# Kernel tuning notes

Hardware: AMD Instinct MI355X
Metric: run time of the kernel (lower is better)

The kernel has to match this reference:

```python
import jax, jax.numpy as jnp
import numpy as np


def _next_pow2(n: int) -> int:
    # matches torch: 2 ** ceil(log2(n))
    return 1 << (int(n) - 1).bit_length()


def setup_inputs() -> dict:
    key = jax.random.key(0)
    k1, k2 = jax.random.split(key)
    B, T, L = 256, 32768, 32768
    x = jax.random.normal(k1, (B, T), dtype=jnp.float32)
    filt = jax.random.normal(k2, (1, L), dtype=jnp.float32)
    return {"x": x, "filt": filt}


def reference(x, filt):
    """EpochedFutureFill.forward: exact causal convolution of x with filt.

    The per-token epoched algorithm (tau-step direct sum + FutureFill FFT
    cache refresh every K steps, cache initialized to zero) computes exactly
    y[b, t] = sum_{s=0}^{min(t, L-1)} filt[0, s] * x[b, t-s].
    We compute it with one FFT-based linear convolution, mirroring the
    float32 FFT math of future_fill().
    """
    B, T = x.shape
    L = filt.shape[-1]
    n_fft = _next_pow2(T + L - 1)
    xf = jnp.fft.rfft(x.astype(jnp.float32), n=n_fft)          # (B, n_fft//2+1)
    wf = jnp.fft.rfft(filt.astype(jnp.float32), n=n_fft)       # (1, n_fft//2+1)
    y = jnp.fft.irfft(xf * wf, n=n_fft)[:, :T]                 # causal lags 0..T-1
    return y.astype(x.dtype)
```

## Files before the change

### kernel.cpp

```cpp
#include <hip/hip_runtime.h>
#include <cstdint>

typedef __attribute__((ext_vector_type(8))) short short8;
typedef __attribute__((ext_vector_type(4))) float floatx4;

#define TWO_PI 6.283185307179586f

__device__ __forceinline__ unsigned short f2bf(float f) {
  union { float f; uint32_t u; } c; c.f = f;
  uint32_t u = c.u;
  u += 0x7FFFu + ((u >> 16) & 1u);
  return (unsigned short)(u >> 16);
}
__device__ __forceinline__ uint32_t packbf(float re, float im) {
  return (uint32_t)f2bf(re) | ((uint32_t)f2bf(im) << 16);
}


__global__ __launch_bounds__(256) void prep_all(
    const float* __restrict__ x, const float* __restrict__ filt,
    unsigned short* __restrict__ A1, unsigned short* __restrict__ A2,
    unsigned short* __restrict__ A3, unsigned short* __restrict__ A4,
    uint32_t* __restrict__ Zp, float2* __restrict__ Gw,
    float2* __restrict__ Tw) {
  __shared__ float2 roots[256];
  const int bid = blockIdx.x;
  const int tid = threadIdx.x;
  const float w256 = TWO_PI / 256.0f;
  if (bid < 3072) {
    if (bid < 512) {
      int j = bid * 256 + tid;
      int jj = j & 7, ln = (j >> 3) & 63, ks = (j >> 9) & 1;
      int t = j >> 10, M16 = t & 31, kc = t >> 5;
      int row = M16 * 16 + (ln & 15);
      int col = kc * 64 + ks * 32 + (ln >> 4) * 8 + jj;
      int k1 = row >> 1, d = row & 1, r = col >> 1, e = col & 1;
      float th = (float)((k1 * r) & 255) * w256;
      float sn, cs; __sincosf(th, &sn, &cs);
      A1[j] = f2bf(d == 0 ? (e == 0 ? cs : sn) : (e == 0 ? -sn : cs));
    } else if (bid < 1536) {
      int j = (bid - 512) * 256 + tid;
      int jj = j & 7, ln = (j >> 3) & 63, ks = (j >> 9) & 1;
      int t = j >> 10, M16 = t & 31, kc = t >> 5;
      int row = M16 * 16 + (ln & 15);
      int col = kc * 64 + ks * 32 + (ln >> 4) * 8 + jj;
      int k2 = row >> 1, d = row & 1, cc = col >> 1, e = col & 1;
      float th = (float)((k2 * cc) & 255) * w256;
      float sn, cs; __sincosf(th, &sn, &cs);
      A2[j] = f2bf(d == 0 ? (e == 0 ? cs : sn) : (e == 0 ? -sn : cs));
    } else if (bid < 2560) {
      int j = (bid - 1536) * 256 + tid;
      int jj = j & 7, ln = (j >> 3) & 63, ks = (j >> 9) & 1;
      int t = j >> 10, M16 = t & 31, kc = t >> 5;
      int row = M16 * 16 + (ln & 15);
      int col = kc * 64 + ks * 32 + (ln >> 4) * 8 + jj;
      int cc = row >> 1, d = row & 1, k2 = col >> 1, e = col & 1;
      float th = (float)((k2 * cc) & 255) * w256;
      float sn, cs; __sincosf(th, &sn, &cs);
      A3[j] = f2bf(d == 0 ? (e == 0 ? cs : -sn) : (e == 0 ? sn : cs));
    } else {
      int j = (bid - 2560) * 256 + tid;
      int jj = j & 7, ln = (j >> 3) & 63, ks = (j >> 9) & 1;
      int t = j >> 10, M16 = t & 15, kc = t >> 4;
      int row = M16 * 16 + (ln & 15);
      int col = kc * 64 + ks * 32 + (ln >> 4) * 8 + jj;
      int r = row >> 1, d = row & 1, k1 = col >> 1, e = col & 1;
      float th = (float)((k1 * r) & 255) * w256;
      float sn, cs; __sincosf(th, &sn, &cs);
      A4[j] = f2bf(d == 0 ? (e == 0 ? cs : -sn) : (e == 0 ? sn : cs));
    }
  } else if (bid < 4096) {
    int b2 = bid - 3072;
    int s = b2 >> 3, rq = b2 & 7;
    const float* x0 = x + (size_t)(2 * s) * 32768;
    const float* x1 = x0 + 32768;
    uint32_t v[16];
    #pragma unroll
    for (int rr = 0; rr < 16; ++rr) {
      int t = tid + 256 * (rq * 16 + rr);
      v[rr] = (uint32_t)f2bf(x0[t]) | ((uint32_t)f2bf(x1[t]) << 16);
    }
    const int kc = rq >> 1, ks = rq & 1;
    uint32_t* dst = Zp + (size_t)s * 32768 +
                    ((kc * 16 + (tid >> 4)) * 2 + ks) * 256 + (tid & 15) * 4;
    #pragma unroll
    for (int q = 0; q < 4; ++q)
      *(uint4*)(dst + q * 64) = make_uint4(v[4*q], v[4*q+1], v[4*q+2], v[4*q+3]);
  } else if (bid < 4352) {
    int k1 = bid - 4096, c = tid;
    { float sn, cs; __sincosf((float)tid * w256, &sn, &cs);
      roots[tid] = make_float2(cs, sn); }
    __syncthreads();
    float ar = 0.f, ai = 0.f;
    for (int r = 0; r < 128; ++r) {
      float v = filt[c + 256 * r];
      float2 wv = roots[(k1 * r) & 255];
      ar += v * wv.x; ai -= v * wv.y;
    }
    float th = (float)((k1 * c) & 65535) * (TWO_PI / 65536.0f);
    float sn, cs; __sincosf(th, &sn, &cs);
    Gw[(k1 << 8) + c] = make_float2(ar * cs + ai * sn, ai * cs - ar * sn);
  } else {
    int k1 = bid - 4352, c = tid;
    float th = (float)((k1 * c) & 65535) * (TWO_PI / 65536.0f);
    float sn, cs; __sincosf(th, &sn, &cs);
    Tw[(k1 << 8) + c] = make_float2(cs, sn);
  }
}

__global__ __launch_bounds__(256) void prep_wb(const float2* __restrict__ Gw,
                                               float2* __restrict__ WtT) {
  __shared__ float2 roots[256];
  int k1 = blockIdx.x, k2 = threadIdx.x;
  { float sn, cs; __sincosf((float)k2 * (TWO_PI / 256.0f), &sn, &cs);
    roots[k2] = make_float2(cs, sn); }
  __syncthreads();
  float ar = 0.f, ai = 0.f;
  for (int c = 0; c < 256; ++c) {
    float2 g = Gw[(k1 << 8) + c];
    float2 wv = roots[(k2 * c) & 255];
    ar += g.x * wv.x + g.y * wv.y;
    ai += g.y * wv.x - g.x * wv.y;
  }
  WtT[(k2 << 8) + k1] = make_float2(ar, ai);
}

template <int MODE, int KC, int MD16>
__global__ __launch_bounds__(256, 2) void dft_stageR(
    const unsigned short* __restrict__ Af,
    const uint32_t* __restrict__ Bf,
    uint32_t* __restrict__ outp,
    float* __restrict__ yout,
    const float2* __restrict__ tab) {
  __shared__ uint32_t Tr[(MODE == 4) ? 64 : 8704];

  const int mt = blockIdx.x >> 8;
  const int nt = blockIdx.x & 255;
  const int m0 = mt * 128, n0 = nt * 128;
  const int s = n0 >> 8;
  const int nlow = n0 & 255;

  const int tid = threadIdx.x;
  const int w = tid >> 6, lane = tid & 63;
  const int qlo = lane & 15, qhi = lane >> 4;
  const int wr = w >> 1, wc = w & 1;

  floatx4 acc[4][4];
  #pragma unroll
  for (int i = 0; i < 4; ++i)
    #pragma unroll
    for (int j = 0; j < 4; ++j) acc[i][j] = (floatx4){0.f, 0.f, 0.f, 0.f};

  const uint32_t* Bp = Bf + (size_t)s * (KC * 8192);
  const int m16b = (m0 >> 4) + wr * 4;
  const int n16b = (nlow >> 4) + wc * 4;

  #pragma unroll
  for (int kc = 0; kc < KC; ++kc) {
    #pragma unroll
    for (int ks = 0; ks < 2; ++ks) {
      short8 a[4], b[4];
      #pragma unroll
      for (int im = 0; im < 4; ++im)
        a[im] = *(const short8*)(Af +
            (size_t)(((kc * MD16 + m16b + im) * 2 + ks) * 512 + lane * 8));
      #pragma unroll
      for (int in = 0; in < 4; ++in)
        b[in] = *(const short8*)(Bp +
            (((kc * 16 + n16b + in) * 2 + ks) * 256 + lane * 4));
      #pragma unroll
      for (int im = 0; im < 4; ++im)
        #pragma unroll
        for (int in = 0; in < 4; ++in)
          acc[im][in] = __builtin_amdgcn_mfma_f32_16x16x32_bf16(
              a[im], b[in], acc[im][in], 0, 0, 0);
    }
  }

  if constexpr (MODE == 1) {
    #pragma unroll
    for (int im = 0; im < 4; ++im) {
      const int mloc = wr * 32 + im * 8 + qhi * 2;
      #pragma unroll
      for (int in = 0; in < 4; ++in) {
        const int nloc = wc * 64 + in * 16 + qlo;
        const int c = nlow + nloc;
        #pragma unroll
        for (int pp = 0; pp < 2; ++pp) {
          const int k1loc = mloc + pp;
          const int k1 = (m0 >> 1) + k1loc;
          float re = acc[im][in][2*pp], iv = acc[im][in][2*pp+1];
          float2 tw = tab[(k1 << 8) + c];
          float r2 = re * tw.x + iv * tw.y, i2 = iv * tw.x - re * tw.y;
          Tr[k1loc * 132 + nloc] = packbf(r2, i2);
        }
      }
    }
    __syncthreads();
    #pragma unroll
    for (int p = 0; p < 8; ++p) {
      const int sb = p * 4 + w;
      const int kcL = sb >> 3, N16l = (sb >> 1) & 3, ksb = sb & 1;
      uint4 v = *(const uint4*)&Tr[(N16l*16 + qlo) * 132 + kcL*32 + ksb*16 + qhi*4];
      const int kcg = (nlow >> 5) + kcL, N16g = (m0 >> 5) + N16l;
      *(uint4*)&outp[(size_t)s * 65536 +
                     (size_t)(((kcg * 16 + N16g) * 2 + ksb) * 256 + lane * 4)] = v;
    }
  } else if constexpr (MODE == 2) {
    #pragma unroll
    for (int im = 0; im < 4; ++im) {
      const int mloc = wr * 32 + im * 8 + qhi * 2;
      #pragma unroll
      for (int in = 0; in < 4; ++in) {
        const int nloc = wc * 64 + in * 16 + qlo;
        const int k1 = nlow + nloc;
        #pragma unroll
        for (int pp = 0; pp < 2; ++pp) {
          const int k2loc = mloc + pp;
          const int k2 = (m0 >> 1) + k2loc;
          float re = acc[im][in][2*pp], iv = acc[im][in][2*pp+1];
          float2 wv = tab[(k2 << 8) + k1];
          float r2 = re * wv.x - iv * wv.y, i2 = re * wv.y + iv * wv.x;
          Tr[nloc * 68 + k2loc] = packbf(r2, i2);
        }
      }
    }
    __syncthreads();
    #pragma unroll
    for (int p = 0; p < 8; ++p) {
      const int sb = p * 4 + w;
      const int kcL = sb >> 4, N16l = (sb >> 1) & 7, ksb = sb & 1;
      uint4 v = *(const uint4*)&Tr[(N16l*16 + qlo) * 68 + kcL*32 + ksb*16 + qhi*4];
      const int kcg = (m0 >> 6) + kcL, N16g = (nlow >> 4) + N16l;
      *(uint4*)&outp[(size_t)s * 65536 +
                     (size_t)(((kcg * 16 + N16g) * 2 + ksb) * 256 + lane * 4)] = v;
    }
  } else if constexpr (MODE == 3) {
    #pragma unroll
    for (int im = 0; im < 4; ++im) {
      const int mloc = wr * 32 + im * 8 + qhi * 2;
      #pragma unroll
      for (int in = 0; in < 4; ++in) {
        const int nloc = wc * 64 + in * 16 + qlo;
        const int k1 = nlow + nloc;
        #pragma unroll
        for (int pp = 0; pp < 2; ++pp) {
          const int cloc = mloc + pp;
          const int c = (m0 >> 1) + cloc;
          float re = acc[im][in][2*pp], iv = acc[im][in][2*pp+1];
          float2 tw = tab[(c << 8) + k1];
          float r2 = re * tw.x - iv * tw.y, i2 = iv * tw.x + re * tw.y;
          Tr[cloc * 132 + nloc] = packbf(r2, i2);
        }
      }
    }
    __syncthreads();
    #pragma unroll
    for (int p = 0; p < 8; ++p) {
      const int sb = p * 4 + w;
      const int kcL = sb >> 3, N16l = (sb >> 1) & 3, ksb = sb & 1;
      uint4 v = *(const uint4*)&Tr[(N16l*16 + qlo) * 132 + kcL*32 + ksb*16 + qhi*4];
      const int kcg = (nlow >> 5) + kcL, N16g = (m0 >> 5) + N16l;
      *(uint4*)&outp[(size_t)s * 65536 +
                     (size_t)(((kcg * 16 + N16g) * 2 + ksb) * 256 + lane * 4)] = v;
    }
  } else {
    #pragma unroll
    for (int im = 0; im < 4; ++im) {
      const int mloc = wr * 32 + im * 8 + qhi * 2;
      #pragma unroll
      for (int in = 0; in < 4; ++in) {
        const int nloc = wc * 64 + in * 16 + qlo;
        const int cloc = nlow + nloc;
        #pragma unroll
        for (int pp = 0; pp < 2; ++pp) {
          const int mC = (m0 >> 1) + mloc + pp;
          float re = acc[im][in][2*pp], iv = acc[im][in][2*pp+1];
          const float sc = 1.0f / 65536.0f;
          float* y0 = yout + ((size_t)s << 16) + (mC << 8) + cloc;
          y0[0] = re * sc;
          y0[32768] = iv * sc;
        }
      }
    }
  }
}

extern "C" void kernel_launch(void* const* d_in, const int* in_sizes, int n_in,
                              void* d_out, int out_size, void* d_ws, size_t ws_size,
                              hipStream_t stream) {
  const float* x = (const float*)d_in[0];
  const float* filt = (const float*)d_in[1];
  float* Y = (float*)d_out;

  char* ws = (char*)d_ws;
  unsigned short* A1 = (unsigned short*)(ws + 0);
  unsigned short* A2 = (unsigned short*)(ws + 0x40000);
  unsigned short* A3 = (unsigned short*)(ws + 0xC0000);
  unsigned short* A4 = (unsigned short*)(ws + 0x140000);
  float2* Gw  = (float2*)(ws + 0x180000);
  float2* WtT = (float2*)(ws + 0x200000);
  float2* Tw  = (float2*)(ws + 0x280000);
  uint32_t* Zp = (uint32_t*)(ws + (3u << 20));
  uint32_t* G2 = (uint32_t*)(ws + 19922944u);
  uint32_t* P  = (uint32_t*)(ws + 53477376u);
  uint32_t* H2 = (uint32_t*)(ws + (3u << 20));

  hipLaunchKernelGGL(prep_all, dim3(4608), dim3(256), 0, stream,
                     x, filt, A1, A2, A3, A4, Zp, Gw, Tw);
  hipLaunchKernelGGL(prep_wb, dim3(256), dim3(256), 0, stream, Gw, WtT);

  hipLaunchKernelGGL((dft_stageR<1, 4, 32>), dim3(1024), dim3(256), 0, stream,
                     A1, Zp, G2, (float*)nullptr, Tw);
  hipLaunchKernelGGL((dft_stageR<2, 8, 32>), dim3(1024), dim3(256), 0, stream,
                     A2, G2, P, (float*)nullptr, WtT);
  hipLaunchKernelGGL((dft_stageR<3, 8, 32>), dim3(1024), dim3(256), 0, stream,
                     A3, P, H2, (float*)nullptr, Tw);
  hipLaunchKernelGGL((dft_stageR<4, 8, 16>), dim3(512), dim3(256), 0, stream,
                     A4, H2, (uint32_t*)nullptr, Y, Tw);
}
```

Before: 197.7 us.

## Fuse DFT stages 2 and 3 into one kernel with LDS-resident intermediate

Merges the second and third matrix-DFT stages into a single kernel. The intermediate P, after its twiddle multiply, now stays in shared memory (64 KB per block) instead of being written to and re-read from global memory. Each 512-thread block handles one quarter of a slice and runs both MFMA GEMMs back to back. This removes one kernel launch and a full round trip of the intermediate through HBM. In exchange it uses large LDS and more registers, which lowers occupancy, and there are fewer blocks (512) to spread across the CUs.

```diff
diff --git a/kernel.cpp b/kernel.cpp
--- a/kernel.cpp
+++ b/kernel.cpp
@@ -206,64 +206,6 @@
       *(uint4*)&outp[(size_t)s * 65536 +
                      (size_t)(((kcg * 16 + N16g) * 2 + ksb) * 256 + lane * 4)] = v;
     }
-  } else if constexpr (MODE == 2) {
-    #pragma unroll
-    for (int im = 0; im < 4; ++im) {
-      const int mloc = wr * 32 + im * 8 + qhi * 2;
-      #pragma unroll
-      for (int in = 0; in < 4; ++in) {
-        const int nloc = wc * 64 + in * 16 + qlo;
-        const int k1 = nlow + nloc;
-        #pragma unroll
-        for (int pp = 0; pp < 2; ++pp) {
-          const int k2loc = mloc + pp;
-          const int k2 = (m0 >> 1) + k2loc;
-          float re = acc[im][in][2*pp], iv = acc[im][in][2*pp+1];
-          float2 wv = tab[(k2 << 8) + k1];
-          float r2 = re * wv.x - iv * wv.y, i2 = re * wv.y + iv * wv.x;
-          Tr[nloc * 68 + k2loc] = packbf(r2, i2);
-        }
-      }
-    }
-    __syncthreads();
-    #pragma unroll
-    for (int p = 0; p < 8; ++p) {
-      const int sb = p * 4 + w;
-      const int kcL = sb >> 4, N16l = (sb >> 1) & 7, ksb = sb & 1;
-      uint4 v = *(const uint4*)&Tr[(N16l*16 + qlo) * 68 + kcL*32 + ksb*16 + qhi*4];
-      const int kcg = (m0 >> 6) + kcL, N16g = (nlow >> 4) + N16l;
-      *(uint4*)&outp[(size_t)s * 65536 +
-                     (size_t)(((kcg * 16 + N16g) * 2 + ksb) * 256 + lane * 4)] = v;
-    }
-  } else if constexpr (MODE == 3) {
-    #pragma unroll
-    for (int im = 0; im < 4; ++im) {
-      const int mloc = wr * 32 + im * 8 + qhi * 2;
-      #pragma unroll
-      for (int in = 0; in < 4; ++in) {
-        const int nloc = wc * 64 + in * 16 + qlo;
-        const int k1 = nlow + nloc;
-        #pragma unroll
-        for (int pp = 0; pp < 2; ++pp) {
-          const int cloc = mloc + pp;
-          const int c = (m0 >> 1) + cloc;
-          float re = acc[im][in][2*pp], iv = acc[im][in][2*pp+1];
-          float2 tw = tab[(c << 8) + k1];
-          float r2 = re * tw.x - iv * tw.y, i2 = iv * tw.x + re * tw.y;
-          Tr[cloc * 132 + nloc] = packbf(r2, i2);
-        }
-      }
-    }
-    __syncthreads();
-    #pragma unroll
-    for (int p = 0; p < 8; ++p) {
-      const int sb = p * 4 + w;
-      const int kcL = sb >> 3, N16l = (sb >> 1) & 3, ksb = sb & 1;
-      uint4 v = *(const uint4*)&Tr[(N16l*16 + qlo) * 132 + kcL*32 + ksb*16 + qhi*4];
-      const int kcg = (nlow >> 5) + kcL, N16g = (m0 >> 5) + N16l;
-      *(uint4*)&outp[(size_t)s * 65536 +
-                     (size_t)(((kcg * 16 + N16g) * 2 + ksb) * 256 + lane * 4)] = v;
-    }
   } else {
     #pragma unroll
     for (int im = 0; im < 4; ++im) {
@@ -281,6 +223,122 @@
           y0[0] = re * sc;
           y0[32768] = iv * sc;
         }
+      }
+    }
+  }
+}
+
+__global__ __launch_bounds__(512, 2) void dft_stage23R(
+    const unsigned short* __restrict__ A2f,
+    const unsigned short* __restrict__ A3f,
+    const uint32_t* __restrict__ G2f,
+    uint32_t* __restrict__ H2f,
+    const float2* __restrict__ WtT,
+    const float2* __restrict__ Tw) {
+  __shared__ uint32_t Pl[16384];
+
+  const int s = blockIdx.x >> 2;
+  const int q = blockIdx.x & 3;
+
+  const int tid = threadIdx.x;
+  const int w = tid >> 6, lane = tid & 63;
+  const int qlo = lane & 15, qhi = lane >> 4;
+  const int wr = w >> 1, wc = w & 1;
+
+  const uint32_t* Bp = G2f + (size_t)s * 65536;
+
+  floatx4 acc[8][2];
+  #pragma unroll
+  for (int i = 0; i < 8; ++i)
+    #pragma unroll
+    for (int j = 0; j < 2; ++j) acc[i][j] = (floatx4){0.f, 0.f, 0.f, 0.f};
+
+  #pragma unroll
+  for (int kc = 0; kc < 8; ++kc) {
+    #pragma unroll
+    for (int ks = 0; ks < 2; ++ks) {
+      short8 b[2];
+      #pragma unroll
+      for (int in = 0; in < 2; ++in) {
+        const int n16 = q * 4 + wc * 2 + in;
+        b[in] = *(const short8*)(Bp + (((kc * 16 + n16) * 2 + ks) * 256 + lane * 4));
+      }
+      #pragma unroll
+      for (int im = 0; im < 8; ++im) {
+        short8 a = *(const short8*)(A2f +
+            (size_t)(((kc * 32 + wr * 8 + im) * 2 + ks) * 512 + lane * 8));
+        #pragma unroll
+        for (int in = 0; in < 2; ++in)
+          acc[im][in] = __builtin_amdgcn_mfma_f32_16x16x32_bf16(
+              a, b[in], acc[im][in], 0, 0, 0);
+      }
+    }
+  }
+
+  #pragma unroll
+  for (int im = 0; im < 8; ++im) {
+    #pragma unroll
+    for (int in = 0; in < 2; ++in) {
+      const int k1l = wc * 32 + in * 16 + qlo;
+      const int k1g = q * 64 + k1l;
+      const int n16l = wc * 2 + in;
+      #pragma unroll
+      for (int pp = 0; pp < 2; ++pp) {
+        const int k2 = (wr * 8 + im) * 8 + qhi * 2 + pp;
+        float re = acc[im][in][2*pp], iv = acc[im][in][2*pp+1];
+        float2 wv = WtT[(k2 << 8) + k1g];
+        float r2 = re * wv.x - iv * wv.y, i2 = re * wv.y + iv * wv.x;
+        const int kcP = k2 >> 5, ksP = (k2 >> 4) & 1;
+        const int qhiP = (k2 >> 2) & 3, jP = k2 & 3;
+        Pl[((kcP * 4 + n16l) * 2 + ksP) * 256 + (qhiP * 16 + qlo) * 4 + jP] =
+            packbf(r2, i2);
+      }
+    }
+  }
+  __syncthreads();
+
+  #pragma unroll
+  for (int i = 0; i < 8; ++i)
+    #pragma unroll
+    for (int j = 0; j < 2; ++j) acc[i][j] = (floatx4){0.f, 0.f, 0.f, 0.f};
+
+  #pragma unroll
+  for (int kc = 0; kc < 8; ++kc) {
+    #pragma unroll
+    for (int ks = 0; ks < 2; ++ks) {
+      short8 b[2];
+      #pragma unroll
+      for (int in = 0; in < 2; ++in)
+        b[in] = *(const short8*)&Pl[((kc * 4 + wc * 2 + in) * 2 + ks) * 256 + lane * 4];
+      #pragma unroll
+      for (int im = 0; im < 8; ++im) {
+        short8 a = *(const short8*)(A3f +
+            (size_t)(((kc * 32 + wr * 8 + im) * 2 + ks) * 512 + lane * 8));
+        #pragma unroll
+        for (int in = 0; in < 2; ++in)
+          acc[im][in] = __builtin_amdgcn_mfma_f32_16x16x32_bf16(
+              a, b[in], acc[im][in], 0, 0, 0);
+      }
+    }
+  }
+
+  uint32_t* Hp = H2f + (size_t)s * 65536;
+  #pragma unroll
+  for (int im = 0; im < 8; ++im) {
+    #pragma unroll
+    for (int in = 0; in < 2; ++in) {
+      const int k1g = q * 64 + wc * 32 + in * 16 + qlo;
+      const int kcH = (q << 1) | wc;
+      const int ksH = in;
+      const int qhiH = qlo >> 2, jH = qlo & 3;
+      #pragma unroll
+      for (int pp = 0; pp < 2; ++pp) {
+        const int c = (wr * 8 + im) * 8 + qhi * 2 + pp;
+        float re = acc[im][in][2*pp], iv = acc[im][in][2*pp+1];
+        float2 tw = Tw[(c << 8) + k1g];
+        float r2 = re * tw.x - iv * tw.y, i2 = iv * tw.x + re * tw.y;
+        Hp[((kcH * 16 + (c >> 4)) * 2 + ksH) * 256 +
+           (qhiH * 16 + (c & 15)) * 4 + jH] = packbf(r2, i2);
       }
     }
   }
@@ -303,8 +361,7 @@
   float2* Tw  = (float2*)(ws + 0x280000);
   uint32_t* Zp = (uint32_t*)(ws + (3u << 20));
   uint32_t* G2 = (uint32_t*)(ws + 19922944u);
-  uint32_t* P  = (uint32_t*)(ws + 53477376u);
-  uint32_t* H2 = (uint32_t*)(ws + (3u << 20));
+  uint32_t* H2 = (uint32_t*)(ws + 53477376u);
 
   hipLaunchKernelGGL(prep_all, dim3(4608), dim3(256), 0, stream,
                      x, filt, A1, A2, A3, A4, Zp, Gw, Tw);
@@ -312,10 +369,8 @@
 
   hipLaunchKernelGGL((dft_stageR<1, 4, 32>), dim3(1024), dim3(256), 0, stream,
                      A1, Zp, G2, (float*)nullptr, Tw);
-  hipLaunchKernelGGL((dft_stageR<2, 8, 32>), dim3(1024), dim3(256), 0, stream,
-                     A2, G2, P, (float*)nullptr, WtT);
-  hipLaunchKernelGGL((dft_stageR<3, 8, 32>), dim3(1024), dim3(256), 0, stream,
-                     A3, P, H2, (float*)nullptr, Tw);
+  hipLaunchKernelGGL(dft_stage23R, dim3(512), dim3(512), 0, stream,
+                     A2, A3, G2, H2, WtT, Tw);
   hipLaunchKernelGGL((dft_stageR<4, 8, 16>), dim3(512), dim3(256), 0, stream,
                      A4, H2, (uint32_t*)nullptr, Y, Tw);
 }
```

New measurement: 277.9 us. +40.6%, slower.
